# Optimization experiments

Measured on AMD Instinct MI355X. Metric: run time of the kernel, lower is better.

The kernel has to match this reference:

```python
import jax, jax.numpy as jnp
import numpy as np

B, H, S, D = 4, 16, 2048, 128

def setup_inputs() -> dict:
    key = jax.random.key(0)
    kq, kk, kv = jax.random.split(key, 3)
    q = jax.random.normal(kq, (B, H, S, D), dtype=jnp.float32)
    k = jax.random.normal(kk, (B, H, S, D), dtype=jnp.float32)
    v = jax.random.normal(kv, (B, H, S, D), dtype=jnp.float32)
    return {"q": q, "k": k, "v": v}

def reference(q, k, v):
    # NOTE: original module applies NO 1/sqrt(d) scale.
    scores = jnp.einsum("bhqd,bhkd->bhqk", q, k)          # [B,H,S,S]
    weights = jax.nn.softmax(scores, axis=-1)
    return jnp.einsum("bhqk,bhkd->bhqd", weights, v)       # [B,H,S,D]
```

## Files before the change

kernel.cpp:

```cpp
#include <hip/hip_runtime.h>
#include <hip/hip_bf16.h>
#include <math.h>
#include <stdint.h>

#define S_LEN 2048
#define D_DIM 128

typedef _Float16 f16x8 __attribute__((ext_vector_type(8)));
typedef __fp16  fp16x2 __attribute__((ext_vector_type(2)));
typedef short bf8_t __attribute__((ext_vector_type(8)));
typedef float f32x4 __attribute__((ext_vector_type(4)));
typedef float f32x16 __attribute__((ext_vector_type(16)));
typedef unsigned int uint32x2 __attribute__((ext_vector_type(2)));
typedef _Float16 f16_t;

__device__ __forceinline__ short f2bf(float f) {
    union { float f; unsigned u; } x; x.f = f;
    unsigned u = x.u;
    u += 0x7FFF + ((u >> 16) & 1);
    return (short)(u >> 16);
}
__device__ __forceinline__ float bf2f(short h) {
    union { unsigned u; float f; } x;
    x.u = ((unsigned)(unsigned short)h) << 16;
    return x.f;
}
__device__ __forceinline__ uint32_t pkf16(float a, float b) {
    union { fp16x2 h; uint32_t u; } x;
    x.h = __builtin_amdgcn_cvt_pkrtz(a, b);
    return x.u;
}
__device__ __forceinline__ uint32x2 plswap(uint32_t a, uint32_t b) {
    return __builtin_amdgcn_permlane32_swap(a, b, false, false);
}
__device__ __forceinline__ float exp2_fast(float x) {
    float r;
    asm("v_exp_f32 %0, %1" : "=v"(r) : "v"(x));
    return r;
}

#define TILE_B 16384
#define WS_VT  33554432u
#define WS_NEED 67108864u

typedef const uint32_t __attribute__((address_space(1))) ga_u32;
typedef uint32_t __attribute__((address_space(3))) la_u32;
__device__ __forceinline__ void gload16(void* l, const void* g) {
    __builtin_amdgcn_global_load_lds((ga_u32*)g, (la_u32*)l, 16, 0, 0);
}

__global__ __launch_bounds__(256, 4)
void conv_kv(const float* __restrict__ K, const float* __restrict__ V,
             char* __restrict__ kf, char* __restrict__ vt)
{
    size_t tile = blockIdx.x;
    const float4* kg = (const float4*)(K + tile * (64 * 128));
    char* kd = kf + tile * TILE_B;
    #pragma unroll
    for (int it = 0; it < 8; ++it) {
        int idx = it * 256 + threadIdx.x;
        int row = idx >> 5;
        int d0  = (idx & 31) * 4;
        float4 kk = kg[idx];
        uint32_t a = pkf16(kk.x, kk.y);
        uint32_t b = pkf16(kk.z, kk.w);
        uint32_t byte = (uint32_t)((row * 256 + d0 * 2) ^ ((row & 15) << 4));
        *(uint32_t*)(kd + byte)     = a;
        *(uint32_t*)(kd + byte + 4) = b;
    }
    const float* vs = V + tile * (64 * 128);
    char* vd = vt + tile * TILE_B;
    #pragma unroll
    for (int it = 0; it < 8; ++it) {
        int idx = it * 256 + threadIdx.x;
        int d  = idx & 127;
        int k0 = (idx >> 7) * 4;
        uint32_t a = pkf16(vs[(k0 + 0) * 128 + d], vs[(k0 + 1) * 128 + d]);
        uint32_t b = pkf16(vs[(k0 + 2) * 128 + d], vs[(k0 + 3) * 128 + d]);
        uint32_t byte = (uint32_t)(((d >> 1) * 256 + (k0 >> 3) * 32 + (d & 1) * 16 + (k0 & 7) * 2)
                                   ^ (((d >> 1) & 15) << 4));
        *(uint32_t*)(vd + byte)     = a;
        *(uint32_t*)(vd + byte + 4) = b;
    }
}

__global__ __launch_bounds__(512, 2)
void attn32(const float* __restrict__ Q, const char* __restrict__ ws,
            float* __restrict__ O)
{
    __shared__ __align__(16) char lds[98304];

    const int tid  = threadIdx.x;
    const int w    = tid >> 6;
    const int lane = tid & 63;
    const int ql   = lane & 31;
    const int h    = lane >> 5;

    const int fid  = blockIdx.x;
    const int nid  = (fid & 7) * 64 + (fid >> 3);
    const int qblk = nid & 7;
    const int bh   = nid >> 3;

    const size_t base = (size_t)bh * S_LEN * D_DIM;
    const int qrow0 = qblk * 256 + w * 32;

    const float L2E = 1.44269504f;
    f16x8 qf[8];
    {
        const float* qp = Q + base + (size_t)(qrow0 + ql) * D_DIM;
        #pragma unroll
        for (int c = 0; c < 8; ++c) {
            const int d0 = c * 16 + h * 8;
            float4 f0 = *(const float4*)(qp + d0);
            float4 f1 = *(const float4*)(qp + d0 + 4);
            qf[c][0] = (f16_t)(f0.x * L2E); qf[c][1] = (f16_t)(f0.y * L2E);
            qf[c][2] = (f16_t)(f0.z * L2E); qf[c][3] = (f16_t)(f0.w * L2E);
            qf[c][4] = (f16_t)(f1.x * L2E); qf[c][5] = (f16_t)(f1.y * L2E);
            qf[c][6] = (f16_t)(f1.z * L2E); qf[c][7] = (f16_t)(f1.w * L2E);
        }
    }
    asm volatile("s_waitcnt vmcnt(0)" ::: "memory");

    f32x16 oacc[4];
    #pragma unroll
    for (int nt = 0; nt < 4; ++nt)
        #pragma unroll
        for (int r = 0; r < 16; ++r) oacc[nt][r] = 0.f;
    float m_run = -INFINITY, l_run = 0.f;

    const char* kf_t = ws + (size_t)(bh * 32) * TILE_B;
    const char* vt_t = ws + WS_VT + (size_t)(bh * 32) * TILE_B;
    const int swk = (ql & 15) << 4;
    const int vbase = (ql >> 1) * 256 + (ql & 1) * 16;
    const int swv = (ql >> 1) << 4;

    #pragma unroll
    for (int tt = 0; tt < 2; ++tt) {
        #pragma unroll
        for (int j = 0; j < 2; ++j) {
            const int off = j * 8192 + w * 1024;
            gload16(lds + tt * 32768 + off,         kf_t + off + lane * 16);
            gload16(lds + tt * 32768 + 16384 + off, vt_t + off + lane * 16);
        }
        kf_t += TILE_B; vt_t += TILE_B;
    }

    int rdb = 0;
    int stb = 65536;
    for (int t6 = 0; t6 < 32; ++t6) {
        if (t6 == 31) { asm volatile("s_waitcnt vmcnt(0)" ::: "memory"); }
        else          { asm volatile("s_waitcnt vmcnt(4)" ::: "memory"); }
        asm volatile("s_barrier" ::: "memory");

        if (t6 < 30) {
            #pragma unroll
            for (int j = 0; j < 2; ++j) {
                const int off = j * 8192 + w * 1024;
                gload16(lds + stb + off,         kf_t + off + lane * 16);
                gload16(lds + stb + 16384 + off, vt_t + off + lane * 16);
            }
            kf_t += TILE_B; vt_t += TILE_B;
            stb = (stb == 65536) ? 0 : stb + 32768;
        }

        f32x16 s0, s1;
        #pragma unroll
        for (int r = 0; r < 16; ++r) { s0[r] = 0.f; s1[r] = 0.f; }
        __builtin_amdgcn_s_setprio(1);
        #pragma unroll
        for (int c = 0; c < 8; ++c) {
            const int b0 = (ql * 256 + c * 32 + h * 16) ^ swk;
            f16x8 a0 = *(const f16x8*)(lds + rdb + b0);
            f16x8 a1 = *(const f16x8*)(lds + rdb + b0 + 8192);
            s0 = __builtin_amdgcn_mfma_f32_32x32x16_f16(a0, qf[c], s0, 0, 0, 0);
            s1 = __builtin_amdgcn_mfma_f32_32x32x16_f16(a1, qf[c], s1, 0, 0, 0);
        }
        __builtin_amdgcn_s_setprio(0);

        float tm = fmaxf(s0[0], s1[0]);
        #pragma unroll
        for (int r = 1; r < 16; ++r)
            tm = fmaxf(tm, fmaxf(s0[r], s1[r]));
        {
            uint32x2 ts = plswap(__float_as_uint(tm), __float_as_uint(tm));
            tm = fmaxf(__uint_as_float(ts[0]), __uint_as_float(ts[1]));
        }
        if (__any(tm > m_run + 11.f)) {
            const float mn = fmaxf(m_run, tm);
            const float sc = exp2_fast(m_run - mn);
            m_run = mn;
            l_run *= sc;
            #pragma unroll
            for (int r = 0; r < 16; ++r) {
                const float scq = __shfl(sc, (r & 3) + 8 * (r >> 2) + 4 * h);
                oacc[0][r] *= scq; oacc[1][r] *= scq;
                oacc[2][r] *= scq; oacc[3][r] *= scq;
            }
        }
        float ps = 0.f;
        #pragma unroll
        for (int r = 0; r < 16; ++r) {
            float p0 = exp2_fast(s0[r] - m_run); s0[r] = p0; ps += p0;
            float p1 = exp2_fast(s1[r] - m_run); s1[r] = p1; ps += p1;
        }
        {
            uint32x2 pss = plswap(__float_as_uint(ps), __float_as_uint(ps));
            ps = __uint_as_float(pss[0]) + __uint_as_float(pss[1]);
        }
        l_run += ps;

        f16x8 pf[4];
        {
            uint32_t pk[8];
            #pragma unroll
            for (int i = 0; i < 8; ++i) pk[i] = pkf16(s0[2 * i], s0[2 * i + 1]);
            uint32x2 r02 = plswap(pk[0], pk[2]), r13 = plswap(pk[1], pk[3]);
            uint32x2 r46 = plswap(pk[4], pk[6]), r57 = plswap(pk[5], pk[7]);
            union { uint32_t u[4]; f16x8 v; } b0, b1;
            b0.u[0] = r02[0]; b0.u[1] = r13[0]; b0.u[2] = r02[1]; b0.u[3] = r13[1];
            b1.u[0] = r46[0]; b1.u[1] = r57[0]; b1.u[2] = r46[1]; b1.u[3] = r57[1];
            pf[0] = b0.v; pf[1] = b1.v;
        }
        {
            uint32_t pk[8];
            #pragma unroll
            for (int i = 0; i < 8; ++i) pk[i] = pkf16(s1[2 * i], s1[2 * i + 1]);
            uint32x2 r02 = plswap(pk[0], pk[2]), r13 = plswap(pk[1], pk[3]);
            uint32x2 r46 = plswap(pk[4], pk[6]), r57 = plswap(pk[5], pk[7]);
            union { uint32_t u[4]; f16x8 v; } b0, b1;
            b0.u[0] = r02[0]; b0.u[1] = r13[0]; b0.u[2] = r02[1]; b0.u[3] = r13[1];
            b1.u[0] = r46[0]; b1.u[1] = r57[0]; b1.u[2] = r46[1]; b1.u[3] = r57[1];
            pf[2] = b0.v; pf[3] = b1.v;
        }

        __builtin_amdgcn_s_setprio(1);
        #pragma unroll
        for (int nt = 0; nt < 4; ++nt) {
            #pragma unroll
            for (int kc = 0; kc < 4; ++kc) {
                const int byte = (nt * 4096 + vbase + (kc * 2 + h) * 32) ^ swv;
                f16x8 vb = *(const f16x8*)(lds + rdb + 16384 + byte);
                oacc[nt] = __builtin_amdgcn_mfma_f32_32x32x16_f16(pf[kc], vb, oacc[nt], 0, 0, 0);
            }
        }
        __builtin_amdgcn_s_setprio(0);

        rdb = (rdb == 65536) ? 0 : rdb + 32768;
    }

    const float inv = 1.f / l_run;
    #pragma unroll
    for (int r = 0; r < 16; ++r) {
        const int qr = (r & 3) + 8 * (r >> 2) + 4 * h;
        const float iv = __shfl(inv, qr);
        float* op = O + base + (size_t)(qrow0 + qr) * D_DIM + ql;
        op[0]  = oacc[0][r] * iv;
        op[32] = oacc[1][r] * iv;
        op[64] = oacc[2][r] * iv;
        op[96] = oacc[3][r] * iv;
    }
}

#define PADK 136
#define PADV 72
#define LDS_SHORTS 31232

__global__ __launch_bounds__(256, 2)
void attn_fwd_fb(const float* __restrict__ Q, const float* __restrict__ K,
                 const float* __restrict__ V, float* __restrict__ O)
{
    __shared__ short lds[LDS_SHORTS];
    short* khi = lds;
    short* klo = lds + 8704;
    short* vt  = lds + 17408;
    short* pls = lds + 26624;

    const int tid  = threadIdx.x;
    const int w    = tid >> 6;
    const int lane = tid & 63;
    const int lg   = lane & 15;
    const int gq   = lane >> 4;
    const int qblk = blockIdx.x;
    const int bh   = blockIdx.y;
    const size_t base = (size_t)bh * S_LEN * D_DIM;
    const int qrow0 = qblk * 64 + w * 16;

    bf8_t qhi[4], qlo[4];
    {
        const float* qp = Q + base + (size_t)(qrow0 + lg) * D_DIM;
        #pragma unroll
        for (int c = 0; c < 4; ++c) {
            const int d0 = c * 32 + gq * 8;
            #pragma unroll
            for (int j = 0; j < 8; ++j) {
                float f = qp[d0 + j];
                short hh = f2bf(f);
                qhi[c][j] = hh;
                qlo[c][j] = f2bf(f - bf2f(hh));
            }
        }
    }

    f32x4 oacc[8];
    #pragma unroll
    for (int n = 0; n < 8; ++n) oacc[n] = (f32x4){0.f, 0.f, 0.f, 0.f};
    float mrow[4] = {-INFINITY, -INFINITY, -INFINITY, -INFINITY};
    float lrow[4] = {0.f, 0.f, 0.f, 0.f};

    for (int kv = 0; kv < S_LEN; kv += 64) {
        __syncthreads();
        {
            const float4* kg = (const float4*)(K + base + (size_t)kv * D_DIM);
            const float4* vg = (const float4*)(V + base + (size_t)kv * D_DIM);
            #pragma unroll
            for (int it = 0; it < 8; ++it) {
                const int f4  = it * 256 + tid;
                const int row = f4 >> 5;
                const int d   = (f4 & 31) * 4;
                float4 kk = kg[f4];
                float4 vv = vg[f4];
                short h0 = f2bf(kk.x), h1 = f2bf(kk.y), h2 = f2bf(kk.z), h3 = f2bf(kk.w);
                short4 hw; hw.x = h0; hw.y = h1; hw.z = h2; hw.w = h3;
                *(short4*)(&khi[row * PADK + d]) = hw;
                short4 lw;
                lw.x = f2bf(kk.x - bf2f(h0));
                lw.y = f2bf(kk.y - bf2f(h1));
                lw.z = f2bf(kk.z - bf2f(h2));
                lw.w = f2bf(kk.w - bf2f(h3));
                *(short4*)(&klo[row * PADK + d]) = lw;
                vt[(d + 0) * PADV + row] = f2bf(vv.x);
                vt[(d + 1) * PADV + row] = f2bf(vv.y);
                vt[(d + 2) * PADV + row] = f2bf(vv.z);
                vt[(d + 3) * PADV + row] = f2bf(vv.w);
            }
        }
        __syncthreads();

        f32x4 sacc[4];
        #pragma unroll
        for (int t = 0; t < 4; ++t) sacc[t] = (f32x4){0.f, 0.f, 0.f, 0.f};
        #pragma unroll
        for (int t = 0; t < 4; ++t) {
            const int krow = t * 16 + lg;
            #pragma unroll
            for (int c = 0; c < 4; ++c) {
                bf8_t kh = *(const bf8_t*)(&khi[krow * PADK + c * 32 + gq * 8]);
                bf8_t kl = *(const bf8_t*)(&klo[krow * PADK + c * 32 + gq * 8]);
                sacc[t] = __builtin_amdgcn_mfma_f32_16x16x32_bf16(qhi[c], kh, sacc[t], 0, 0, 0);
                sacc[t] = __builtin_amdgcn_mfma_f32_16x16x32_bf16(qlo[c], kh, sacc[t], 0, 0, 0);
                sacc[t] = __builtin_amdgcn_mfma_f32_16x16x32_bf16(qhi[c], kl, sacc[t], 0, 0, 0);
            }
        }

        float scl[4];
        #pragma unroll
        for (int r = 0; r < 4; ++r) {
            float tm = fmaxf(fmaxf(sacc[0][r], sacc[1][r]),
                             fmaxf(sacc[2][r], sacc[3][r]));
            #pragma unroll
            for (int off = 8; off >= 1; off >>= 1)
                tm = fmaxf(tm, __shfl_xor(tm, off, 64));
            const float mn = fmaxf(mrow[r], tm);
            const float sc = __expf(mrow[r] - mn);
            float ps = 0.f;
            #pragma unroll
            for (int t = 0; t < 4; ++t) {
                float p = __expf(sacc[t][r] - mn);
                sacc[t][r] = p;
                ps += p;
            }
            #pragma unroll
            for (int off = 8; off >= 1; off >>= 1)
                ps += __shfl_xor(ps, off, 64);
            lrow[r] = lrow[r] * sc + ps;
            mrow[r] = mn;
            scl[r] = sc;
        }
        #pragma unroll
        for (int n = 0; n < 8; ++n) {
            oacc[n][0] *= scl[0];
            oacc[n][1] *= scl[1];
            oacc[n][2] *= scl[2];
            oacc[n][3] *= scl[3];
        }

        short* pw = pls + w * (16 * PADV);
        #pragma unroll
        for (int t = 0; t < 4; ++t)
            #pragma unroll
            for (int r = 0; r < 4; ++r)
                pw[(gq * 4 + r) * PADV + t * 16 + lg] = f2bf(sacc[t][r]);
        asm volatile("s_waitcnt lgkmcnt(0)" ::: "memory");

        #pragma unroll
        for (int kt = 0; kt < 2; ++kt) {
            bf8_t pa = *(const bf8_t*)(&pw[lg * PADV + kt * 32 + gq * 8]);
            #pragma unroll
            for (int n = 0; n < 8; ++n) {
                bf8_t vb = *(const bf8_t*)(&vt[(n * 16 + lg) * PADV + kt * 32 + gq * 8]);
                oacc[n] = __builtin_amdgcn_mfma_f32_16x16x32_bf16(pa, vb, oacc[n], 0, 0, 0);
            }
        }
    }

    float inv[4];
    #pragma unroll
    for (int r = 0; r < 4; ++r) inv[r] = 1.f / lrow[r];
    float* op = O + base + (size_t)qrow0 * D_DIM;
    #pragma unroll
    for (int n = 0; n < 8; ++n)
        #pragma unroll
        for (int r = 0; r < 4; ++r)
            op[(size_t)(gq * 4 + r) * D_DIM + n * 16 + lg] = oacc[n][r] * inv[r];
}

extern "C" void kernel_launch(void* const* d_in, const int* in_sizes, int n_in,
                              void* d_out, int out_size, void* d_ws, size_t ws_size,
                              hipStream_t stream) {
    const float* q = (const float*)d_in[0];
    const float* k = (const float*)d_in[1];
    const float* v = (const float*)d_in[2];
    float* o = (float*)d_out;
    if (ws_size >= (size_t)WS_NEED) {
        char* ws = (char*)d_ws;
        conv_kv<<<2048, 256, 0, stream>>>(k, v, ws, ws + WS_VT);
        attn32<<<512, 512, 0, stream>>>(q, ws, o);
    } else {
        attn_fwd_fb<<<dim3(32, 64), 256, 0, stream>>>(q, k, v, o);
    }
}
```

Before: 212.3 us.

## Software-pipeline QK^T of next tile with softmax and PV of previous tile

Restructures the attention loop so that the QK^T MFMAs for tile t are issued while the softmax and PV product run on the scores of tile t-1, which are held in extra registers. LDS staging grows from three to four K/V buffers, with three tiles prefetched up front, so the previous tile's V stays resident while new tiles stream in. A peeled prologue computes the first tile's scores and an epilogue finishes the last tile. The aim is to hide the exp and max latency behind matrix-core work. The cost is 32 more live accumulator registers, which risks spills or lower occupancy, plus a larger LDS footprint.

```diff
diff --git a/kernel.cpp b/kernel.cpp
--- a/kernel.cpp
+++ b/kernel.cpp
@@ -88,7 +88,7 @@
 void attn32(const float* __restrict__ Q, const char* __restrict__ ws,
             float* __restrict__ O)
 {
-    __shared__ __align__(16) char lds[98304];
+    __shared__ __align__(16) char lds[131072];
 
     const int tid  = threadIdx.x;
     const int w    = tid >> 6;
@@ -135,7 +135,7 @@
     const int swv = (ql >> 1) << 4;
 
     #pragma unroll
-    for (int tt = 0; tt < 2; ++tt) {
+    for (int tt = 0; tt < 3; ++tt) {
         #pragma unroll
         for (int j = 0; j < 2; ++j) {
             const int off = j * 8192 + w * 1024;
@@ -144,15 +144,34 @@
         }
         kf_t += TILE_B; vt_t += TILE_B;
     }
-
-    int rdb = 0;
-    int stb = 65536;
-    for (int t6 = 0; t6 < 32; ++t6) {
+    asm volatile("s_waitcnt vmcnt(8)" ::: "memory");
+    asm volatile("s_barrier" ::: "memory");
+
+    f32x16 s0p, s1p;
+    {
+        #pragma unroll
+        for (int r = 0; r < 16; ++r) { s0p[r] = 0.f; s1p[r] = 0.f; }
+        __builtin_amdgcn_s_setprio(1);
+        #pragma unroll
+        for (int c = 0; c < 8; ++c) {
+            const int b0 = (ql * 256 + c * 32 + h * 16) ^ swk;
+            f16x8 a0 = *(const f16x8*)(lds + b0);
+            f16x8 a1 = *(const f16x8*)(lds + b0 + 8192);
+            s0p = __builtin_amdgcn_mfma_f32_32x32x16_f16(a0, qf[c], s0p, 0, 0, 0);
+            s1p = __builtin_amdgcn_mfma_f32_32x32x16_f16(a1, qf[c], s1p, 0, 0, 0);
+        }
+        __builtin_amdgcn_s_setprio(0);
+    }
+
+    int rdb = 32768;
+    int rdp = 0;
+    int stb = 98304;
+    for (int t6 = 1; t6 < 32; ++t6) {
         if (t6 == 31) { asm volatile("s_waitcnt vmcnt(0)" ::: "memory"); }
         else          { asm volatile("s_waitcnt vmcnt(4)" ::: "memory"); }
         asm volatile("s_barrier" ::: "memory");
 
-        if (t6 < 30) {
+        if (t6 <= 29) {
             #pragma unroll
             for (int j = 0; j < 2; ++j) {
                 const int off = j * 8192 + w * 1024;
@@ -160,7 +179,7 @@
                 gload16(lds + stb + 16384 + off, vt_t + off + lane * 16);
             }
             kf_t += TILE_B; vt_t += TILE_B;
-            stb = (stb == 65536) ? 0 : stb + 32768;
+            stb = (stb == 98304) ? 0 : stb + 32768;
         }
 
         f32x16 s0, s1;
@@ -177,10 +196,10 @@
         }
         __builtin_amdgcn_s_setprio(0);
 
-        float tm = fmaxf(s0[0], s1[0]);
+        float tm = fmaxf(s0p[0], s1p[0]);
         #pragma unroll
         for (int r = 1; r < 16; ++r)
-            tm = fmaxf(tm, fmaxf(s0[r], s1[r]));
+            tm = fmaxf(tm, fmaxf(s0p[r], s1p[r]));
         {
             uint32x2 ts = plswap(__float_as_uint(tm), __float_as_uint(tm));
             tm = fmaxf(__uint_as_float(ts[0]), __uint_as_float(ts[1]));
@@ -200,8 +219,8 @@
         float ps = 0.f;
         #pragma unroll
         for (int r = 0; r < 16; ++r) {
-            float p0 = exp2_fast(s0[r] - m_run); s0[r] = p0; ps += p0;
-            float p1 = exp2_fast(s1[r] - m_run); s1[r] = p1; ps += p1;
+            float p0 = exp2_fast(s0p[r] - m_run); s0p[r] = p0; ps += p0;
+            float p1 = exp2_fast(s1p[r] - m_run); s1p[r] = p1; ps += p1;
         }
         {
             uint32x2 pss = plswap(__float_as_uint(ps), __float_as_uint(ps));
@@ -213,7 +232,7 @@
         {
             uint32_t pk[8];
             #pragma unroll
-            for (int i = 0; i < 8; ++i) pk[i] = pkf16(s0[2 * i], s0[2 * i + 1]);
+            for (int i = 0; i < 8; ++i) pk[i] = pkf16(s0p[2 * i], s0p[2 * i + 1]);
             uint32x2 r02 = plswap(pk[0], pk[2]), r13 = plswap(pk[1], pk[3]);
             uint32x2 r46 = plswap(pk[4], pk[6]), r57 = plswap(pk[5], pk[7]);
             union { uint32_t u[4]; f16x8 v; } b0, b1;
@@ -224,7 +243,7 @@
         {
             uint32_t pk[8];
             #pragma unroll
-            for (int i = 0; i < 8; ++i) pk[i] = pkf16(s1[2 * i], s1[2 * i + 1]);
+            for (int i = 0; i < 8; ++i) pk[i] = pkf16(s1p[2 * i], s1p[2 * i + 1]);
             uint32x2 r02 = plswap(pk[0], pk[2]), r13 = plswap(pk[1], pk[3]);
             uint32x2 r46 = plswap(pk[4], pk[6]), r57 = plswap(pk[5], pk[7]);
             union { uint32_t u[4]; f16x8 v; } b0, b1;
@@ -239,13 +258,86 @@
             #pragma unroll
             for (int kc = 0; kc < 4; ++kc) {
                 const int byte = (nt * 4096 + vbase + (kc * 2 + h) * 32) ^ swv;
-                f16x8 vb = *(const f16x8*)(lds + rdb + 16384 + byte);
+                f16x8 vb = *(const f16x8*)(lds + rdp + 16384 + byte);
                 oacc[nt] = __builtin_amdgcn_mfma_f32_32x32x16_f16(pf[kc], vb, oacc[nt], 0, 0, 0);
             }
         }
         __builtin_amdgcn_s_setprio(0);
 
-        rdb = (rdb == 65536) ? 0 : rdb + 32768;
+        #pragma unroll
+        for (int r = 0; r < 16; ++r) { s0p[r] = s0[r]; s1p[r] = s1[r]; }
+        rdp = rdb;
+        rdb = (rdb == 98304) ? 0 : rdb + 32768;
+    }
+
+    {
+        float tm = fmaxf(s0p[0], s1p[0]);
+        #pragma unroll
+        for (int r = 1; r < 16; ++r)
+            tm = fmaxf(tm, fmaxf(s0p[r], s1p[r]));
+        {
+            uint32x2 ts = plswap(__float_as_uint(tm), __float_as_uint(tm));
+            tm = fmaxf(__uint_as_float(ts[0]), __uint_as_float(ts[1]));
+        }
+        if (__any(tm > m_run + 11.f)) {
+            const float mn = fmaxf(m_run, tm);
+            const float sc = exp2_fast(m_run - mn);
+            m_run = mn;
+            l_run *= sc;
+            #pragma unroll
+            for (int r = 0; r < 16; ++r) {
+                const float scq = __shfl(sc, (r & 3) + 8 * (r >> 2) + 4 * h);
+                oacc[0][r] *= scq; oacc[1][r] *= scq;
+                oacc[2][r] *= scq; oacc[3][r] *= scq;
+            }
+        }
+        float ps = 0.f;
+        #pragma unroll
+        for (int r = 0; r < 16; ++r) {
+            float p0 = exp2_fast(s0p[r] - m_run); s0p[r] = p0; ps += p0;
+            float p1 = exp2_fast(s1p[r] - m_run); s1p[r] = p1; ps += p1;
+        }
+        {
+            uint32x2 pss = plswap(__float_as_uint(ps), __float_as_uint(ps));
+            ps = __uint_as_float(pss[0]) + __uint_as_float(pss[1]);
+        }
+        l_run += ps;
+
+        f16x8 pf[4];
+        {
+            uint32_t pk[8];
+            #pragma unroll
+            for (int i = 0; i < 8; ++i) pk[i] = pkf16(s0p[2 * i], s0p[2 * i + 1]);
+            uint32x2 r02 = plswap(pk[0], pk[2]), r13 = plswap(pk[1], pk[3]);
+            uint32x2 r46 = plswap(pk[4], pk[6]), r57 = plswap(pk[5], pk[7]);
+            union { uint32_t u[4]; f16x8 v; } b0, b1;
+            b0.u[0] = r02[0]; b0.u[1] = r13[0]; b0.u[2] = r02[1]; b0.u[3] = r13[1];
+            b1.u[0] = r46[0]; b1.u[1] = r57[0]; b1.u[2] = r46[1]; b1.u[3] = r57[1];
+            pf[0] = b0.v; pf[1] = b1.v;
+        }
+        {
+            uint32_t pk[8];
+            #pragma unroll
+            for (int i = 0; i < 8; ++i) pk[i] = pkf16(s1p[2 * i], s1p[2 * i + 1]);
+            uint32x2 r02 = plswap(pk[0], pk[2]), r13 = plswap(pk[1], pk[3]);
+            uint32x2 r46 = plswap(pk[4], pk[6]), r57 = plswap(pk[5], pk[7]);
+            union { uint32_t u[4]; f16x8 v; } b0, b1;
+            b0.u[0] = r02[0]; b0.u[1] = r13[0]; b0.u[2] = r02[1]; b0.u[3] = r13[1];
+            b1.u[0] = r46[0]; b1.u[1] = r57[0]; b1.u[2] = r46[1]; b1.u[3] = r57[1];
+            pf[2] = b0.v; pf[3] = b1.v;
+        }
+
+        __builtin_amdgcn_s_setprio(1);
+        #pragma unroll
+        for (int nt = 0; nt < 4; ++nt) {
+            #pragma unroll
+            for (int kc = 0; kc < 4; ++kc) {
+                const int byte = (nt * 4096 + vbase + (kc * 2 + h) * 32) ^ swv;
+                f16x8 vb = *(const f16x8*)(lds + rdp + 16384 + byte);
+                oacc[nt] = __builtin_amdgcn_mfma_f32_32x32x16_f16(pf[kc], vb, oacc[nt], 0, 0, 0);
+            }
+        }
+        __builtin_amdgcn_s_setprio(0);
     }
 
     const float inv = 1.f / l_run;
```

After: 213.9 us. Within noise of the previous version (+0.7%).
